# Kernel tuning notes

Hardware: AMD Instinct MI355X
Metric: run time of the kernel (lower is better)

The kernel has to match this reference:

```python
import jax, jax.numpy as jnp
import numpy as np

CH = 512
HEADS = 4
GROUPS = 32  # _groups(512) -> 32
EPS = 1e-5


def setup_inputs() -> dict:
    key = jax.random.key(0)
    ks = jax.random.split(key, 7)
    b, c, h, w = 16, CH, 32, 32
    sd = 1.0 / np.sqrt(c)
    return {
        "x": jax.random.normal(ks[0], (b, c, h, w), dtype=jnp.float32),
        "gamma": jnp.ones((c,), jnp.float32),
        "beta": jnp.zeros((c,), jnp.float32),
        "w_qkv": jax.random.normal(ks[1], (3 * c, c), dtype=jnp.float32) * sd,
        "b_qkv": jax.random.normal(ks[2], (3 * c,), dtype=jnp.float32) * 0.01,
        "w_proj": jax.random.normal(ks[3], (c, c), dtype=jnp.float32) * sd,
        "b_proj": jax.random.normal(ks[4], (c,), dtype=jnp.float32) * 0.01,
    }


def _group_norm(x, gamma, beta):
    b, c, h, w = x.shape
    xg = x.reshape(b, GROUPS, -1)  # (b, G, c//G * h * w)
    mu = jnp.mean(xg, axis=-1, keepdims=True)
    var = jnp.var(xg, axis=-1, keepdims=True)
    xn = ((xg - mu) * jax.lax.rsqrt(var + EPS)).reshape(b, c, h, w)
    return xn * gamma[None, :, None, None] + beta[None, :, None, None]


def reference(x, gamma, beta, w_qkv, b_qkv, w_proj, b_proj):
    b, c, h, w = x.shape
    hd = c // HEADS
    xn = _group_norm(x, gamma, beta)
    # 1x1 conv == channel matmul
    qkv = jnp.einsum('oc,bchw->bohw', w_qkv, xn) + b_qkv[None, :, None, None]
    qkv = qkv.reshape(b, 3, HEADS, hd, h * w)
    q, k, v = qkv[:, 0], qkv[:, 1], qkv[:, 2]  # (b, H, hd, n)
    scale = hd ** -0.5
    attn = jax.nn.softmax(jnp.einsum('bhcn,bhcm->bhnm', q * scale, k), axis=-1)
    out = jnp.einsum('bhnm,bhcm->bhcn', attn, v).reshape(b, c, h, w)
    out = jnp.einsum('oc,bchw->bohw', w_proj, out) + b_proj[None, :, None, None]
    return x + out
```

## Files before the change

kernel.cpp:

```cpp
#include <hip/hip_runtime.h>

#define CH 512
#define HEADS 4
#define HD 128
#define NPIX 1024
#define BATCH 16
#define GROUPS 32
#define GSZ 16
#define EPS 1e-5f

typedef _Float16 f16;
typedef _Float16 f16x8 __attribute__((ext_vector_type(8)));
typedef _Float16 f16x4 __attribute__((ext_vector_type(4)));
typedef float f32x4 __attribute__((ext_vector_type(4)));

__device__ __forceinline__ void gld16(const f16* g, f16* l) {
    __builtin_amdgcn_global_load_lds((__attribute__((address_space(1))) const void*)g,
                                     (__attribute__((address_space(3))) void*)l, 16, 0, 0);
}

__global__ void k_convert(const float* __restrict__ wq, const float* __restrict__ wp,
                          f16* __restrict__ wqT, f16* __restrict__ wpT) {
    int c = blockIdx.x * 256 + threadIdx.x;
    {
        int ot = c >> 13, kbl = (c >> 7) & 63, ol = c & 127;
        const float* s = wq + ((size_t)(ot * 128 + ol)) * CH + kbl * 8;
        f32x4 a = *(const f32x4*)s, b = *(const f32x4*)(s + 4);
        f16x8 v;
        v[0] = (f16)a.x; v[1] = (f16)a.y; v[2] = (f16)a.z; v[3] = (f16)a.w;
        v[4] = (f16)b.x; v[5] = (f16)b.y; v[6] = (f16)b.z; v[7] = (f16)b.w;
        *(f16x8*)(wqT + (size_t)c * 8) = v;
    }
    if (c < 32768) {
        int ot = c >> 13, kbl = (c >> 7) & 63, ol = c & 127;
        const float* s = wp + ((size_t)(ot * 128 + ol)) * CH + kbl * 8;
        f32x4 a = *(const f32x4*)s, b = *(const f32x4*)(s + 4);
        f16x8 v;
        v[0] = (f16)a.x; v[1] = (f16)a.y; v[2] = (f16)a.z; v[3] = (f16)a.w;
        v[4] = (f16)b.x; v[5] = (f16)b.y; v[6] = (f16)b.z; v[7] = (f16)b.w;
        *(f16x8*)(wpT + (size_t)c * 8) = v;
    }
}

__global__ __launch_bounds__(256, 2) void k_gn(const float* __restrict__ x, const float* __restrict__ gamma,
                                               const float* __restrict__ beta, f16* __restrict__ xnT) {
    int g = blockIdx.x, b = blockIdx.y;
    __shared__ float xs[GSZ * NPIX];
    __shared__ float red[8];
    __shared__ float stat2[2];
    const f32x4* x4 = (const f32x4*)(x + ((size_t)(b * GROUPS + g)) * (GSZ * NPIX));
    float s = 0.f, ss = 0.f;
    for (int i = threadIdx.x; i < GSZ * NPIX / 4; i += 256) {
        f32x4 v = x4[i];
        *(f32x4*)&xs[i * 4] = v;
        s  += v.x + v.y + v.z + v.w;
        ss += v.x * v.x + v.y * v.y + v.z * v.z + v.w * v.w;
    }
    for (int off = 32; off; off >>= 1) { s += __shfl_down(s, off); ss += __shfl_down(ss, off); }
    int wv = threadIdx.x >> 6, ln = threadIdx.x & 63;
    if (ln == 0) { red[wv] = s; red[4 + wv] = ss; }
    __syncthreads();
    if (threadIdx.x == 0) {
        float S = red[0] + red[1] + red[2] + red[3];
        float SS = red[4] + red[5] + red[6] + red[7];
        float mu = S / (GSZ * NPIX);
        float var = SS / (GSZ * NPIX) - mu * mu;
        stat2[0] = mu; stat2[1] = rsqrtf(var + EPS);
    }
    __syncthreads();
    float mu = stat2[0], rstd = stat2[1];
    int ch = threadIdx.x >> 7;
    int n  = threadIdx.x & 127;
    float gl[8], bl[8];
#pragma unroll
    for (int i = 0; i < 8; i++) {
        float gv = gamma[g * 16 + ch * 8 + i] * rstd;
        gl[i] = gv;
        bl[i] = beta[g * 16 + ch * 8 + i] - mu * gv;
    }
    f16* tb0 = xnT + ((size_t)(b * 8)) * 65536 + (g * 2 + ch) * 1024 + n * 8;
#pragma unroll
    for (int nt = 0; nt < 8; nt++) {
        f16x8 o;
#pragma unroll
        for (int i = 0; i < 8; i++)
            o[i] = (f16)(xs[(ch * 8 + i) * 1024 + nt * 128 + n] * gl[i] + bl[i]);
        *(f16x8*)(tb0 + (size_t)nt * 65536) = o;
    }
}

__global__ __launch_bounds__(256, 3) void k_qkv(const f16* __restrict__ wT, const float* __restrict__ bias,
                                                const f16* __restrict__ xnT, f16* __restrict__ qF,
                                                f16* __restrict__ kTl, f16* __restrict__ vTl) {
    int nt = blockIdx.x, ot = blockIdx.y, b = blockIdx.z;
    int o0 = ot * 128;
    __shared__ union SM {
        struct { f16 As[8192]; f16 Bs[8192]; } s;
        f16 Cf[16384];
    } sm;
    __shared__ float biasS[128];
    if (threadIdx.x < 128) biasS[threadIdx.x] = bias[o0 + threadIdx.x];
    int tid = threadIdx.x, lane = tid & 63, wv = tid >> 6;
    int wr = wv >> 1, wc = wv & 1;
    int l15 = lane & 15, quad = lane >> 4;
    const f16* wA = wT + (size_t)ot * 65536;
    const f16* xB = xnT + ((size_t)(b * 8 + nt)) * 65536;
    f32x4 acc[4][4] = {};
    for (int kk = 0; kk < CH; kk += 64) {
        __syncthreads();
        const f16* sa = wA + (size_t)(kk >> 3) * 1024;
        const f16* sb = xB + (size_t)(kk >> 3) * 1024;
#pragma unroll
        for (int i = 0; i < 4; i++) {
            int s = wv * 4 + i;
            gld16(sa + (size_t)(s * 64 + lane) * 8, sm.s.As + s * 512);
            gld16(sb + (size_t)(s * 64 + lane) * 8, sm.s.Bs + s * 512);
        }
        __syncthreads();
#pragma unroll
        for (int dk = 0; dk < 2; dk++) {
            f16x8 af[4], bf[4];
#pragma unroll
            for (int t = 0; t < 4; t++) {
                af[t] = *(const f16x8*)(sm.s.As + (dk * 4 + quad) * 1024 + (wr * 64 + t * 16 + l15) * 8);
                bf[t] = *(const f16x8*)(sm.s.Bs + (dk * 4 + quad) * 1024 + (wc * 64 + t * 16 + l15) * 8);
            }
#pragma unroll
            for (int tm = 0; tm < 4; tm++)
#pragma unroll
                for (int tn = 0; tn < 4; tn++)
                    acc[tm][tn] = __builtin_amdgcn_mfma_f32_16x16x32_f16(af[tm], bf[tn], acc[tm][tn], 0, 0, 0);
        }
    }
    __syncthreads();
    int which = ot >> 2, h = ot & 3;
#pragma unroll
    for (int tm = 0; tm < 4; tm++)
#pragma unroll
        for (int tn = 0; tn < 4; tn++) {
            int ob = wr * 64 + tm * 16 + quad * 4;
            int n  = wc * 64 + tn * 16 + l15;
            f16x4 pv;
#pragma unroll
            for (int r = 0; r < 4; r++) pv[r] = (f16)(acc[tm][tn][r] + biasS[ob + r]);
            if (which == 0) {
                int addr = ((((n >> 5) * 2 + ((n >> 4) & 1)) * 4 + (ob >> 5)) * 512)
                         + ((ob >> 3) & 3) * 128 + (n & 15) * 8 + (quad & 1) * 4;
                *(f16x4*)&sm.Cf[addr] = pv;
            } else if (which == 1) {
                int addr = (ob >> 3) * 1024 + n * 8 + (quad & 1) * 4;
                *(f16x4*)&sm.Cf[addr] = pv;
            } else {
#pragma unroll
                for (int r = 0; r < 4; r++)
                    sm.Cf[(n >> 3) * 1024 + (ob + r) * 8 + (n & 7)] = pv[r];
            }
        }
    __syncthreads();
    f16* tb = (which == 0) ? (qF + ((size_t)((b * 4 + h) * 8 + nt)) * 16384)
            : (which == 1) ? (kTl + ((size_t)((b * 4 + h) * 8 + nt)) * 16384)
                           : (vTl + ((size_t)((b * 4 + h) * 8 + nt)) * 16384);
#pragma unroll
    for (int i = 0; i < 8; i++) {
        int cid = tid + i * 256;
        *(f16x8*)(tb + (size_t)cid * 8) = *(const f16x8*)(sm.Cf + cid * 8);
    }
}

__global__ __launch_bounds__(512, 1) void k_attn(const f16* __restrict__ qF, const f16* __restrict__ kTl,
                                                 const f16* __restrict__ vTl, f16* __restrict__ oT) {
    int bid = blockIdx.x;
    int ntp = bid >> 6, group = bid & 63;
    int b = group >> 2, h = group & 3;
    extern __shared__ f16 smem[];
    f16* Kl = smem;
    f16* Vl = smem + 16384;
    f16* PA = smem + 32768;
    f16* PB = smem + 49152;
    int tid = threadIdx.x, lane = tid & 63, wv = tid >> 6;
    int wq = wv & 3;
    int tile = wv >> 2;
    int nt = ntp * 2 + tile;
    int l15 = lane & 15, quad = lane >> 4;
    const f16* qb = qF + ((size_t)(group * 8 + nt)) * 16384;
    const f16* kb = kTl + (size_t)group * 8 * 16384;
    const f16* vb = vTl + (size_t)group * 8 * 16384;
    f16* Preg = tile ? PB : PA;

    f16x8 aq[2][4];
#pragma unroll
    for (int t = 0; t < 2; t++)
#pragma unroll
        for (int dk = 0; dk < 4; dk++) {
            int seg = (wq * 2 + t) * 4 + dk;
            f16x8 v = *(const f16x8*)(qb + seg * 512 + lane * 8);
            aq[t][dk] = v * (f16)0.08838834764831845f;
        }

    float m_i[2] = {-1e30f, -1e30f}, l_i[2] = {0.f, 0.f};
    f32x4 oaccT[2][8] = {};

    const f16* sbase = tile ? vb : kb;
    f16* dstL = tile ? Vl : Kl;
    f16x8 buf[8];
#pragma unroll
    for (int i = 0; i < 8; i++)
        buf[i] = *(const f16x8*)(sbase + (size_t)((wq * 8 + i) * 64 + lane) * 8);

    for (int mc = 0; mc < 8; mc++) {
        __syncthreads();
#pragma unroll
        for (int i = 0; i < 8; i++)
            *(f16x8*)&dstL[(wq * 8 + i) * 512 + lane * 8] = buf[i];
        __syncthreads();

        f32x4 st[2][8] = {};
#pragma unroll
        for (int dk = 0; dk < 4; dk++) {
            f16x8 kf[8];
#pragma unroll
            for (int t = 0; t < 8; t++)
                kf[t] = *(const f16x8*)&Kl[(dk * 4 + quad) * 1024 + (t * 16 + l15) * 8];
#pragma unroll
            for (int tr = 0; tr < 2; tr++)
#pragma unroll
                for (int tc = 0; tc < 8; tc++)
                    st[tr][tc] = __builtin_amdgcn_mfma_f32_16x16x32_f16(kf[tc], aq[tr][dk], st[tr][tc], 0, 0, 0);
        }

#pragma unroll
        for (int tr = 0; tr < 2; tr++) {
            float a[8];
#pragma unroll
            for (int tc = 0; tc < 8; tc++)
                a[tc] = fmaxf(fmaxf(st[tr][tc][0], st[tr][tc][1]), fmaxf(st[tr][tc][2], st[tr][tc][3]));
#pragma unroll
            for (int s = 4; s; s >>= 1)
#pragma unroll
                for (int k = 0; k < 4; k++) if (k < s) a[k] = fmaxf(a[k], a[k + s]);
            float mx = a[0];
            mx = fmaxf(mx, __shfl_xor(mx, 16));
            mx = fmaxf(mx, __shfl_xor(mx, 32));
            float mnew = fmaxf(m_i[tr], mx);
            float alpha = __expf(m_i[tr] - mnew);
            m_i[tr] = mnew;
            float r4[8];
#pragma unroll
            for (int tc = 0; tc < 8; tc++) {
                float p0 = __expf(st[tr][tc][0] - mnew);
                float p1 = __expf(st[tr][tc][1] - mnew);
                float p2 = __expf(st[tr][tc][2] - mnew);
                float p3 = __expf(st[tr][tc][3] - mnew);
                st[tr][tc][0] = p0; st[tr][tc][1] = p1;
                st[tr][tc][2] = p2; st[tr][tc][3] = p3;
                r4[tc] = (p0 + p1) + (p2 + p3);
            }
#pragma unroll
            for (int s = 4; s; s >>= 1)
#pragma unroll
                for (int k = 0; k < 4; k++) if (k < s) r4[k] += r4[k + s];
            float rs = r4[0];
            rs += __shfl_xor(rs, 16);
            rs += __shfl_xor(rs, 32);
            l_i[tr] = l_i[tr] * alpha + rs;
#pragma unroll
            for (int tc = 0; tc < 8; tc++) {
                oaccT[tr][tc].x *= alpha; oaccT[tr][tc].y *= alpha;
                oaccT[tr][tc].z *= alpha; oaccT[tr][tc].w *= alpha;
            }
        }

#pragma unroll
        for (int tr = 0; tr < 2; tr++) {
            int n = wq * 32 + tr * 16 + l15;
#pragma unroll
            for (int tc = 0; tc < 8; tc++) {
                int blk = tc * 2 + (quad >> 1);
                f16x4 pv;
#pragma unroll
                for (int r = 0; r < 4; r++) pv[r] = (f16)st[tr][tc][r];
                *(f16x4*)&Preg[n * 128 + ((blk ^ (n & 15)) << 3) + ((quad & 1) << 2)] = pv;
            }
        }

        if (mc < 7) {
            const f16* s = sbase + (size_t)(mc + 1) * 16384;
#pragma unroll
            for (int i = 0; i < 8; i++)
                buf[i] = *(const f16x8*)(s + (size_t)((wq * 8 + i) * 64 + lane) * 8);
        }

#pragma unroll
        for (int mk = 0; mk < 4; mk++) {
            f16x8 vf[8], pf[2];
#pragma unroll
            for (int t = 0; t < 8; t++)
                vf[t] = *(const f16x8*)&Vl[(mk * 4 + quad) * 1024 + (t * 16 + l15) * 8];
#pragma unroll
            for (int tr = 0; tr < 2; tr++) {
                int n = wq * 32 + tr * 16 + l15;
                int blk = mk * 4 + quad;
                pf[tr] = *(const f16x8*)&Preg[n * 128 + ((blk ^ (n & 15)) << 3)];
            }
#pragma unroll
            for (int tr = 0; tr < 2; tr++)
#pragma unroll
                for (int tc = 0; tc < 8; tc++)
                    oaccT[tr][tc] = __builtin_amdgcn_mfma_f32_16x16x32_f16(vf[tc], pf[tr], oaccT[tr][tc], 0, 0, 0);
        }
    }

#pragma unroll
    for (int tr = 0; tr < 2; tr++) {
        float inv = 1.f / l_i[tr];
        int n = wq * 32 + tr * 16 + l15;
#pragma unroll
        for (int tc = 0; tc < 8; tc++) {
            int blk = tc * 2 + (quad >> 1);
            f16x4 ov;
#pragma unroll
            for (int r = 0; r < 4; r++) ov[r] = (f16)(oaccT[tr][tc][r] * inv);
            *(f16x4*)&Preg[n * 128 + ((blk ^ (n & 15)) << 3) + ((quad & 1) << 2)] = ov;
        }
    }
    __syncthreads();
    f16* ob = oT + ((size_t)(b * 8 + nt)) * 65536;
    int t256 = tid & 255;
#pragma unroll
    for (int i = 0; i < 8; i++) {
        int cid = t256 + i * 256;
        int cbl = cid >> 7, n = cid & 127;
        f16x8 v = *(const f16x8*)&Preg[n * 128 + ((cbl ^ (n & 15)) << 3)];
        *(f16x8*)(ob + (size_t)(h * 16 + cbl) * 1024 + n * 8) = v;
    }
}

__global__ __launch_bounds__(256, 3) void k_proj(const f16* __restrict__ wT, const float* __restrict__ bias,
                                                 const f16* __restrict__ oT, const float* __restrict__ x,
                                                 float* __restrict__ out) {
    int nt = blockIdx.x, ot = blockIdx.y, b = blockIdx.z;
    int n0 = nt * 128, o0 = ot * 128;
    __shared__ union SM {
        struct { f16 As[8192]; f16 Bs[8192]; } s;
        f16 Cs[128][136];
    } sm;
    __shared__ float biasS[128];
    if (threadIdx.x < 128) biasS[threadIdx.x] = bias[o0 + threadIdx.x];
    int tid = threadIdx.x, lane = tid & 63, wv = tid >> 6;
    int wr = wv >> 1, wc = wv & 1;
    int l15 = lane & 15, quad = lane >> 4;
    const f16* wA = wT + (size_t)ot * 65536;
    const f16* xB = oT + ((size_t)(b * 8 + nt)) * 65536;
    f32x4 acc[4][4] = {};
    for (int kk = 0; kk < CH; kk += 64) {
        __syncthreads();
        const f16* sa = wA + (size_t)(kk >> 3) * 1024;
        const f16* sb = xB + (size_t)(kk >> 3) * 1024;
#pragma unroll
        for (int i = 0; i < 4; i++) {
            int s = wv * 4 + i;
            gld16(sa + (size_t)(s * 64 + lane) * 8, sm.s.As + s * 512);
            gld16(sb + (size_t)(s * 64 + lane) * 8, sm.s.Bs + s * 512);
        }
        __syncthreads();
#pragma unroll
        for (int dk = 0; dk < 2; dk++) {
            f16x8 af[4], bf[4];
#pragma unroll
            for (int t = 0; t < 4; t++) {
                af[t] = *(const f16x8*)(sm.s.As + (dk * 4 + quad) * 1024 + (wr * 64 + t * 16 + l15) * 8);
                bf[t] = *(const f16x8*)(sm.s.Bs + (dk * 4 + quad) * 1024 + (wc * 64 + t * 16 + l15) * 8);
            }
#pragma unroll
            for (int tm = 0; tm < 4; tm++)
#pragma unroll
                for (int tn = 0; tn < 4; tn++)
                    acc[tm][tn] = __builtin_amdgcn_mfma_f32_16x16x32_f16(af[tm], bf[tn], acc[tm][tn], 0, 0, 0);
        }
    }
    __syncthreads();
#pragma unroll
    for (int tm = 0; tm < 4; tm++)
#pragma unroll
        for (int tn = 0; tn < 4; tn++)
#pragma unroll
            for (int r = 0; r < 4; r++) {
                int o = wr * 64 + tm * 16 + quad * 4 + r;
                int n = wc * 64 + tn * 16 + l15;
                sm.Cs[o][n] = (f16)(acc[tm][tn][r] + biasS[o]);
            }
    __syncthreads();
#pragma unroll
    for (int i = 0; i < 8; i++) {
        int cid = tid + i * 256;
        int row = cid >> 4, off = (cid & 15) * 8;
        f16x8 v = *(const f16x8*)&sm.Cs[row][off];
        size_t gofs = ((size_t)(b * CH) + o0 + row) * NPIX + n0 + off;
        const float* xp = x + gofs;
        float* op = out + gofs;
        f32x4 o0v, o1v;
        o0v.x = xp[0] + (float)v[0]; o0v.y = xp[1] + (float)v[1];
        o0v.z = xp[2] + (float)v[2]; o0v.w = xp[3] + (float)v[3];
        o1v.x = xp[4] + (float)v[4]; o1v.y = xp[5] + (float)v[5];
        o1v.z = xp[6] + (float)v[6]; o1v.w = xp[7] + (float)v[7];
        *(f32x4*)op = o0v; *(f32x4*)(op + 4) = o1v;
    }
}

extern "C" void kernel_launch(void* const* d_in, const int* in_sizes, int n_in,
                              void* d_out, int out_size, void* d_ws, size_t ws_size,
                              hipStream_t stream) {
    const float* x     = (const float*)d_in[0];
    const float* gamma = (const float*)d_in[1];
    const float* beta  = (const float*)d_in[2];
    const float* wqkv  = (const float*)d_in[3];
    const float* bqkv  = (const float*)d_in[4];
    const float* wproj = (const float*)d_in[5];
    const float* bproj = (const float*)d_in[6];
    float* out = (float*)d_out;

    char* p = (char*)d_ws;
    f16* wqT = (f16*)p;           p += (size_t)3 * CH * CH * 2;
    f16* wpT = (f16*)p;           p += (size_t)CH * CH * 2;
    f16* xnT = (f16*)p;           p += (size_t)BATCH * NPIX * CH * 2;
    f16* qF  = (f16*)p;           p += (size_t)BATCH * HEADS * NPIX * HD * 2;
    f16* kTl = (f16*)p;           p += (size_t)BATCH * HEADS * NPIX * HD * 2;
    f16* vTl = (f16*)p;           p += (size_t)BATCH * HEADS * NPIX * HD * 2;
    f16* oT  = (f16*)p;           p += (size_t)BATCH * NPIX * CH * 2;

    k_convert<<<dim3(384), 256, 0, stream>>>(wqkv, wproj, wqT, wpT);
    k_gn<<<dim3(GROUPS, BATCH), 256, 0, stream>>>(x, gamma, beta, xnT);
    k_qkv<<<dim3(8, 12, BATCH), 256, 0, stream>>>(wqT, bqkv, xnT, qF, kTl, vTl);

    hipFuncSetAttribute((const void*)k_attn, hipFuncAttributeMaxDynamicSharedMemorySize, 131072);
    k_attn<<<dim3(256), 512, 131072, stream>>>(qF, kTl, vTl, oT);

    k_proj<<<dim3(8, 4, BATCH), 256, 0, stream>>>(wpT, bproj, oT, x, out);
}
```

Before: 202.5 us.

## Merge weight conversion into group-norm kernel and widen QKV tiles to 128x256

Folds the fp32-to-fp16 weight conversion into the group-norm launch as extra blocks, removing one kernel launch and letting the two independent jobs overlap. The QKV GEMM block now covers two pixel tiles (256 columns), so each loaded weight tile is reused twice. This halves the grid and doubles the accumulator registers, and occupancy drops from 3 to 2 blocks per CU. The epilogue writes the two halves in turn through the shared staging buffer.

```diff
diff --git a/kernel.cpp b/kernel.cpp
--- a/kernel.cpp
+++ b/kernel.cpp
@@ -19,35 +19,37 @@
                                      (__attribute__((address_space(3))) void*)l, 16, 0, 0);
 }
 
-__global__ void k_convert(const float* __restrict__ wq, const float* __restrict__ wp,
-                          f16* __restrict__ wqT, f16* __restrict__ wpT) {
-    int c = blockIdx.x * 256 + threadIdx.x;
-    {
-        int ot = c >> 13, kbl = (c >> 7) & 63, ol = c & 127;
-        const float* s = wq + ((size_t)(ot * 128 + ol)) * CH + kbl * 8;
-        f32x4 a = *(const f32x4*)s, b = *(const f32x4*)(s + 4);
-        f16x8 v;
-        v[0] = (f16)a.x; v[1] = (f16)a.y; v[2] = (f16)a.z; v[3] = (f16)a.w;
-        v[4] = (f16)b.x; v[5] = (f16)b.y; v[6] = (f16)b.z; v[7] = (f16)b.w;
-        *(f16x8*)(wqT + (size_t)c * 8) = v;
-    }
-    if (c < 32768) {
-        int ot = c >> 13, kbl = (c >> 7) & 63, ol = c & 127;
-        const float* s = wp + ((size_t)(ot * 128 + ol)) * CH + kbl * 8;
-        f32x4 a = *(const f32x4*)s, b = *(const f32x4*)(s + 4);
-        f16x8 v;
-        v[0] = (f16)a.x; v[1] = (f16)a.y; v[2] = (f16)a.z; v[3] = (f16)a.w;
-        v[4] = (f16)b.x; v[5] = (f16)b.y; v[6] = (f16)b.z; v[7] = (f16)b.w;
-        *(f16x8*)(wpT + (size_t)c * 8) = v;
-    }
-}
-
-__global__ __launch_bounds__(256, 2) void k_gn(const float* __restrict__ x, const float* __restrict__ gamma,
-                                               const float* __restrict__ beta, f16* __restrict__ xnT) {
-    int g = blockIdx.x, b = blockIdx.y;
+__global__ __launch_bounds__(256, 2) void k_pre(const float* __restrict__ x, const float* __restrict__ gamma,
+                                                const float* __restrict__ beta, f16* __restrict__ xnT,
+                                                const float* __restrict__ wq, const float* __restrict__ wp,
+                                                f16* __restrict__ wqT, f16* __restrict__ wpT) {
     __shared__ float xs[GSZ * NPIX];
     __shared__ float red[8];
     __shared__ float stat2[2];
+    int bidx = blockIdx.x;
+    if (bidx >= 512) {
+        int c = (bidx - 512) * 256 + threadIdx.x;
+        {
+            int ot = c >> 13, kbl = (c >> 7) & 63, ol = c & 127;
+            const float* s = wq + ((size_t)(ot * 128 + ol)) * CH + kbl * 8;
+            f32x4 a = *(const f32x4*)s, b2 = *(const f32x4*)(s + 4);
+            f16x8 v;
+            v[0] = (f16)a.x; v[1] = (f16)a.y; v[2] = (f16)a.z; v[3] = (f16)a.w;
+            v[4] = (f16)b2.x; v[5] = (f16)b2.y; v[6] = (f16)b2.z; v[7] = (f16)b2.w;
+            *(f16x8*)(wqT + (size_t)c * 8) = v;
+        }
+        if (c < 32768) {
+            int ot = c >> 13, kbl = (c >> 7) & 63, ol = c & 127;
+            const float* s = wp + ((size_t)(ot * 128 + ol)) * CH + kbl * 8;
+            f32x4 a = *(const f32x4*)s, b2 = *(const f32x4*)(s + 4);
+            f16x8 v;
+            v[0] = (f16)a.x; v[1] = (f16)a.y; v[2] = (f16)a.z; v[3] = (f16)a.w;
+            v[4] = (f16)b2.x; v[5] = (f16)b2.y; v[6] = (f16)b2.z; v[7] = (f16)b2.w;
+            *(f16x8*)(wpT + (size_t)c * 8) = v;
+        }
+        return;
+    }
+    int g = bidx & 31, b = bidx >> 5;
     const f32x4* x4 = (const f32x4*)(x + ((size_t)(b * GROUPS + g)) * (GSZ * NPIX));
     float s = 0.f, ss = 0.f;
     for (int i = threadIdx.x; i < GSZ * NPIX / 4; i += 256) {
@@ -89,13 +91,13 @@
     }
 }
 
-__global__ __launch_bounds__(256, 3) void k_qkv(const f16* __restrict__ wT, const float* __restrict__ bias,
+__global__ __launch_bounds__(256, 2) void k_qkv(const f16* __restrict__ wT, const float* __restrict__ bias,
                                                 const f16* __restrict__ xnT, f16* __restrict__ qF,
                                                 f16* __restrict__ kTl, f16* __restrict__ vTl) {
-    int nt = blockIdx.x, ot = blockIdx.y, b = blockIdx.z;
+    int ntp = blockIdx.x, ot = blockIdx.y, b = blockIdx.z;
     int o0 = ot * 128;
     __shared__ union SM {
-        struct { f16 As[8192]; f16 Bs[8192]; } s;
+        struct { f16 As[8192]; f16 Bs[16384]; } s;
         f16 Cf[16384];
     } sm;
     __shared__ float biasS[128];
@@ -104,66 +106,79 @@
     int wr = wv >> 1, wc = wv & 1;
     int l15 = lane & 15, quad = lane >> 4;
     const f16* wA = wT + (size_t)ot * 65536;
-    const f16* xB = xnT + ((size_t)(b * 8 + nt)) * 65536;
-    f32x4 acc[4][4] = {};
+    const f16* xB0 = xnT + ((size_t)(b * 8 + ntp * 2)) * 65536;
+    const f16* xB1 = xnT + ((size_t)(b * 8 + ntp * 2 + 1)) * 65536;
+    f32x4 acc[4][8] = {};
     for (int kk = 0; kk < CH; kk += 64) {
         __syncthreads();
         const f16* sa = wA + (size_t)(kk >> 3) * 1024;
-        const f16* sb = xB + (size_t)(kk >> 3) * 1024;
-#pragma unroll
-        for (int i = 0; i < 4; i++) {
-            int s = wv * 4 + i;
-            gld16(sa + (size_t)(s * 64 + lane) * 8, sm.s.As + s * 512);
-            gld16(sb + (size_t)(s * 64 + lane) * 8, sm.s.Bs + s * 512);
+#pragma unroll
+        for (int i = 0; i < 12; i++) {
+            int sid = wv * 12 + i;
+            if (sid < 16) {
+                gld16(sa + (size_t)(sid * 64 + lane) * 8, sm.s.As + sid * 512);
+            } else {
+                int t = sid - 16;
+                int kbl = t >> 2, half = (t >> 1) & 1, sub = t & 1;
+                const f16* src = (half ? xB1 : xB0) + (size_t)((kk >> 3) + kbl) * 1024 + (size_t)(sub * 64 + lane) * 8;
+                gld16(src, sm.s.Bs + kbl * 2048 + half * 1024 + sub * 512);
+            }
         }
         __syncthreads();
 #pragma unroll
         for (int dk = 0; dk < 2; dk++) {
-            f16x8 af[4], bf[4];
-#pragma unroll
-            for (int t = 0; t < 4; t++) {
+            f16x8 af[4], bf[8];
+#pragma unroll
+            for (int t = 0; t < 4; t++)
                 af[t] = *(const f16x8*)(sm.s.As + (dk * 4 + quad) * 1024 + (wr * 64 + t * 16 + l15) * 8);
-                bf[t] = *(const f16x8*)(sm.s.Bs + (dk * 4 + quad) * 1024 + (wc * 64 + t * 16 + l15) * 8);
-            }
+#pragma unroll
+            for (int t = 0; t < 8; t++)
+                bf[t] = *(const f16x8*)(sm.s.Bs + (dk * 4 + quad) * 2048 + (wc * 128 + t * 16 + l15) * 8);
 #pragma unroll
             for (int tm = 0; tm < 4; tm++)
 #pragma unroll
-                for (int tn = 0; tn < 4; tn++)
+                for (int tn = 0; tn < 8; tn++)
                     acc[tm][tn] = __builtin_amdgcn_mfma_f32_16x16x32_f16(af[tm], bf[tn], acc[tm][tn], 0, 0, 0);
         }
     }
-    __syncthreads();
     int which = ot >> 2, h = ot & 3;
 #pragma unroll
-    for (int tm = 0; tm < 4; tm++)
-#pragma unroll
-        for (int tn = 0; tn < 4; tn++) {
-            int ob = wr * 64 + tm * 16 + quad * 4;
-            int n  = wc * 64 + tn * 16 + l15;
-            f16x4 pv;
-#pragma unroll
-            for (int r = 0; r < 4; r++) pv[r] = (f16)(acc[tm][tn][r] + biasS[ob + r]);
-            if (which == 0) {
-                int addr = ((((n >> 5) * 2 + ((n >> 4) & 1)) * 4 + (ob >> 5)) * 512)
-                         + ((ob >> 3) & 3) * 128 + (n & 15) * 8 + (quad & 1) * 4;
-                *(f16x4*)&sm.Cf[addr] = pv;
-            } else if (which == 1) {
-                int addr = (ob >> 3) * 1024 + n * 8 + (quad & 1) * 4;
-                *(f16x4*)&sm.Cf[addr] = pv;
-            } else {
-#pragma unroll
-                for (int r = 0; r < 4; r++)
-                    sm.Cf[(n >> 3) * 1024 + (ob + r) * 8 + (n & 7)] = pv[r];
-            }
-        }
-    __syncthreads();
-    f16* tb = (which == 0) ? (qF + ((size_t)((b * 4 + h) * 8 + nt)) * 16384)
-            : (which == 1) ? (kTl + ((size_t)((b * 4 + h) * 8 + nt)) * 16384)
-                           : (vTl + ((size_t)((b * 4 + h) * 8 + nt)) * 16384);
-#pragma unroll
-    for (int i = 0; i < 8; i++) {
-        int cid = tid + i * 256;
-        *(f16x8*)(tb + (size_t)cid * 8) = *(const f16x8*)(sm.Cf + cid * 8);
+    for (int half = 0; half < 2; half++) {
+        __syncthreads();
+        if (wc == half) {
+#pragma unroll
+            for (int tm = 0; tm < 4; tm++)
+#pragma unroll
+                for (int tn = 0; tn < 8; tn++) {
+                    int ob = wr * 64 + tm * 16 + quad * 4;
+                    int n  = tn * 16 + l15;
+                    f16x4 pv;
+#pragma unroll
+                    for (int r = 0; r < 4; r++) pv[r] = (f16)(acc[tm][tn][r] + biasS[ob + r]);
+                    if (which == 0) {
+                        int addr = ((((n >> 5) * 2 + ((n >> 4) & 1)) * 4 + (ob >> 5)) * 512)
+                                 + ((ob >> 3) & 3) * 128 + (n & 15) * 8 + (quad & 1) * 4;
+                        *(f16x4*)&sm.Cf[addr] = pv;
+                    } else if (which == 1) {
+                        int addr = (ob >> 3) * 1024 + n * 8 + (quad & 1) * 4;
+                        *(f16x4*)&sm.Cf[addr] = pv;
+                    } else {
+#pragma unroll
+                        for (int r = 0; r < 4; r++)
+                            sm.Cf[(n >> 3) * 1024 + (ob + r) * 8 + (n & 7)] = pv[r];
+                    }
+                }
+        }
+        __syncthreads();
+        int nt = ntp * 2 + half;
+        f16* tb = (which == 0) ? (qF + ((size_t)((b * 4 + h) * 8 + nt)) * 16384)
+                : (which == 1) ? (kTl + ((size_t)((b * 4 + h) * 8 + nt)) * 16384)
+                               : (vTl + ((size_t)((b * 4 + h) * 8 + nt)) * 16384);
+#pragma unroll
+        for (int i = 0; i < 8; i++) {
+            int cid = tid + i * 256;
+            *(f16x8*)(tb + (size_t)cid * 8) = *(const f16x8*)(sm.Cf + cid * 8);
+        }
     }
 }
 
@@ -428,9 +443,8 @@
     f16* vTl = (f16*)p;           p += (size_t)BATCH * HEADS * NPIX * HD * 2;
     f16* oT  = (f16*)p;           p += (size_t)BATCH * NPIX * CH * 2;
 
-    k_convert<<<dim3(384), 256, 0, stream>>>(wqkv, wproj, wqT, wpT);
-    k_gn<<<dim3(GROUPS, BATCH), 256, 0, stream>>>(x, gamma, beta, xnT);
-    k_qkv<<<dim3(8, 12, BATCH), 256, 0, stream>>>(wqT, bqkv, xnT, qF, kTl, vTl);
+    k_pre<<<dim3(896), 256, 0, stream>>>(x, gamma, beta, xnT, wqkv, wproj, wqT, wpT);
+    k_qkv<<<dim3(4, 12, BATCH), 256, 0, stream>>>(wqT, bqkv, xnT, qF, kTl, vTl);
 
     hipFuncSetAttribute((const void*)k_attn, hipFuncAttributeMaxDynamicSharedMemorySize, 131072);
     k_attn<<<dim3(256), 512, 131072, stream>>>(qF, kTl, vTl, oT);
```

Measured after the change: 211.7 us. +4.6%, slower.
